# Optimization experiments

Measured on AMD Instinct MI355X. Metric: run time of the kernel, lower is better.

## Reference

```python
import jax, jax.numpy as jnp
import numpy as np

NPOINT = 2048
RADIUS = 0.2
NSAMPLE = 64
BN_EPS = 1e-5
MLP = [131, 128, 128, 256]  # 128 features + 3 xyz -> 128 -> 128 -> 256


def fps(xyz, npoint):
    """Furthest point sampling. xyz: (B,N,3) -> inds (B,npoint) int32. First index is 0 (CUDA convention)."""
    B, N, _ = xyz.shape
    dist0 = jnp.full((B, N), 1e10, dtype=xyz.dtype)
    idx0 = jnp.zeros((B,), dtype=jnp.int32)

    def step(carry, _):
        dist, last = carry
        last_pt = jnp.take_along_axis(xyz, last[:, None, None].astype(jnp.int32), axis=1)  # (B,1,3)
        d = jnp.sum((xyz - last_pt) ** 2, axis=-1)  # (B,N)
        dist = jnp.minimum(dist, d)
        nxt = jnp.argmax(dist, axis=1).astype(jnp.int32)
        return (dist, nxt), nxt

    (_, _), rest = jax.lax.scan(step, (dist0, idx0), None, length=npoint - 1)
    return jnp.concatenate([idx0[None, :], rest], axis=0).T  # (B,npoint)


def ball_query(all_xyz, new_xyz, radius, nsample):
    """For each query pick the first (lowest-index) nsample points within radius; pad with first hit.
    all_xyz: (B,Np,3), new_xyz: (B,S,3) -> idx (B,S,nsample) int32."""
    Np = all_xyz.shape[1]
    d2 = jnp.sum((new_xyz[:, :, None, :] - all_xyz[:, None, :, :]) ** 2, axis=-1)  # (B,S,Np)
    key = jnp.where(d2 < radius * radius, jnp.arange(Np, dtype=jnp.int32)[None, None, :], Np)
    topk = -jax.lax.top_k(-key, nsample)[0]  # nsample smallest indices, ascending
    valid = topk < Np
    first = topk[..., :1]
    idx = jnp.where(valid, topk, first)
    return jnp.where(idx >= Np, 0, idx).astype(jnp.int32)


def bn_relu(x, gamma, beta):
    # training-mode BatchNorm over (B,S,K) per channel (last axis), biased variance
    mean = jnp.mean(x, axis=(0, 1, 2), keepdims=True)
    var = jnp.mean((x - mean) ** 2, axis=(0, 1, 2), keepdims=True)
    return jax.nn.relu((x - mean) * jax.lax.rsqrt(var + BN_EPS) * gamma + beta)


def setup_inputs() -> dict:
    key = jax.random.key(0)
    ks = jax.random.split(key, 10)
    B, N, M, C = 4, 16384, 256, 128
    fixed_xyz = jax.random.uniform(ks[0], (B, M, 3), dtype=jnp.float32)
    xyz = jax.random.uniform(ks[1], (B, N, 3), dtype=jnp.float32)
    features = jax.random.normal(ks[2], (B, C, M + N), dtype=jnp.float32)
    W1 = jax.random.normal(ks[3], (MLP[1], MLP[0]), dtype=jnp.float32) * 0.05
    W2 = jax.random.normal(ks[4], (MLP[2], MLP[1]), dtype=jnp.float32) * 0.05
    W3 = jax.random.normal(ks[5], (MLP[3], MLP[2]), dtype=jnp.float32) * 0.05
    g1 = jnp.ones((MLP[1],), jnp.float32); b1 = jnp.zeros((MLP[1],), jnp.float32)
    g2 = jnp.ones((MLP[2],), jnp.float32); b2 = jnp.zeros((MLP[2],), jnp.float32)
    g3 = jnp.ones((MLP[3],), jnp.float32); b3 = jnp.zeros((MLP[3],), jnp.float32)
    return {"fixed_xyz": fixed_xyz, "xyz": xyz, "features": features,
            "W1": W1, "g1": g1, "b1": b1, "W2": W2, "g2": g2, "b2": b2,
            "W3": W3, "g3": g3, "b3": b3}


def reference(fixed_xyz, xyz, features, W1, g1, b1, W2, g2, b2, W3, g3, b3):
    B = xyz.shape[0]
    # FPS on the raw cloud, gather sampled centers, prepend fixed seeds
    inds = fps(xyz, NPOINT)  # (B,npoint)
    sampled = jnp.take_along_axis(xyz, inds[:, :, None], axis=1)  # (B,npoint,3)
    new_xyz = jnp.concatenate([fixed_xyz, sampled], axis=1)       # (B,S,3)
    all_xyz = jnp.concatenate([fixed_xyz, xyz], axis=1)           # (B,Np,3)

    idx = ball_query(all_xyz, new_xyz, RADIUS, NSAMPLE)           # (B,S,K)
    b = jnp.arange(B)[:, None, None]
    grouped_xyz = all_xyz[b, idx] - new_xyz[:, :, None, :]        # (B,S,K,3)
    grouped_xyz = grouped_xyz / RADIUS                            # normalize_xyz=True
    feats_t = jnp.transpose(features, (0, 2, 1))                  # (B,Np,C)
    grouped_feats = feats_t[b, idx]                               # (B,S,K,C)
    h = jnp.concatenate([grouped_xyz, grouped_feats], axis=-1)    # (B,S,K,3+C)

    # Shared MLP: 1x1 conv (no bias) + BN + ReLU per layer
    h = bn_relu(jnp.einsum('bskc,oc->bsko', h, W1), g1, b1)
    h = bn_relu(jnp.einsum('bskc,oc->bsko', h, W2), g2, b2)
    h = bn_relu(jnp.einsum('bskc,oc->bsko', h, W3), g3, b3)

    # max pool over the K (nsample) axis -> (B,Cout,S)
    new_features = jnp.transpose(jnp.max(h, axis=2), (0, 2, 1))
    return new_xyz, new_features, inds
```

## Files before the change

kernel.cpp:

```cpp
#include <hip/hip_runtime.h>
#include <hip/hip_bf16.h>
#include <cstdint>
#include <cstddef>

#define NB 4
#define N_PTS 16384
#define M_FIX 256
#define P_ALL 16640
#define S_TOT 2304
#define NPT 2048
#define KNB 64
#define CH1 128
#define CH3 256
#define NRED 589824.0f

typedef float v2f __attribute__((ext_vector_type(2)));

#define OUT_XYZ 0
#define OUT_FEAT 27648
#define OUT_INDS 2386944

#define OFF_ALLX   0ull
#define OFF_STATS  798720ull
#define OFF_BN     1060864ull
#define OFF_MAXZ   1064960ull
#define OFF_MINZ   10502144ull
#define OFF_IDX    19939328ull
#define OFF_ZP     22298624ull
#define OFF_NEWX   39337984ull
#define OFF_INDSI  39448576ull
#define OFF_HIST   1064960ull
#define OFF_OFFS   1073152ull
#define OFF_SX     1081344ull
#define OFF_SY     1343488ull
#define OFF_SZ     1605632ull
#define OFF_SIDX   1867776ull
#define OFF_XYZ4   2129920ull

__device__ __forceinline__ float red16s(float v) {
  v += __shfl_xor(v, 1); v += __shfl_xor(v, 2);
  v += __shfl_xor(v, 4); v += __shfl_xor(v, 8);
  return v;
}
__device__ __forceinline__ float red16mx(float v) {
  v = fmaxf(v, __shfl_xor(v, 1)); v = fmaxf(v, __shfl_xor(v, 2));
  v = fmaxf(v, __shfl_xor(v, 4)); v = fmaxf(v, __shfl_xor(v, 8));
  return v;
}
__device__ __forceinline__ float red16mn(float v) {
  v = fminf(v, __shfl_xor(v, 1)); v = fminf(v, __shfl_xor(v, 2));
  v = fminf(v, __shfl_xor(v, 4)); v = fminf(v, __shfl_xor(v, 8));
  return v;
}
__device__ __forceinline__ float xyzp(float dx, float dy, float dz,
                                      float wx, float wy, float wz) {
  return fmaf(dx, wx, fmaf(dy, wy, __fmul_rn(dz, wz)));
}
__device__ __forceinline__ int mort3(int v) {
  return (v & 1) | ((v & 2) << 1) | ((v & 4) << 2);
}
__device__ __forceinline__ int cell_code(float x, float y, float z) {
  int cx = min(7, max(0, (int)(x * 8.0f)));
  int cy = min(7, max(0, (int)(y * 8.0f)));
  int cz = min(7, max(0, (int)(z * 8.0f)));
  return mort3(cx) | (mort3(cy) << 1) | (mort3(cz) << 2);
}

template <int CTRL, int RM>
__device__ __forceinline__ unsigned long long dppmax(unsigned long long k) {
  int lo = (int)(unsigned)(k & 0xFFFFFFFFull);
  int hi = (int)(unsigned)(k >> 32);
  int sl = __builtin_amdgcn_update_dpp(lo, lo, CTRL, RM, 0xF, false);
  int sh = __builtin_amdgcn_update_dpp(hi, hi, CTRL, RM, 0xF, false);
  unsigned long long s = ((unsigned long long)(unsigned)sh << 32) | (unsigned)sl;
  return (s > k) ? s : k;
}
__device__ __forceinline__ unsigned long long wave_max64(unsigned long long k) {
  k = dppmax<0x111, 0xF>(k);
  k = dppmax<0x112, 0xF>(k);
  k = dppmax<0x114, 0xF>(k);
  k = dppmax<0x118, 0xF>(k);
  k = dppmax<0x142, 0xa>(k);
  k = dppmax<0x143, 0xc>(k);
  return k;
}
__device__ __forceinline__ unsigned long long row_max64(unsigned long long k) {
  k = dppmax<0x111, 0xF>(k);
  k = dppmax<0x112, 0xF>(k);
  k = dppmax<0x114, 0xF>(k);
  k = dppmax<0x118, 0xF>(k);
  return k;
}

__global__ void k_build(const float* __restrict__ fixed, const float* __restrict__ xyz,
                        float* __restrict__ allx, float* __restrict__ newx,
                        float* __restrict__ stats, int* __restrict__ inds_i,
                        int* __restrict__ hist, float4* __restrict__ xyz4) {
  int i = blockIdx.x * 256 + threadIdx.x;
  if (i < NB * P_ALL * 3) {
    int b = i / (P_ALL * 3);
    int r = i % (P_ALL * 3);
    int p = r / 3, c = r % 3;
    float v = (p < M_FIX) ? fixed[((size_t)b * M_FIX + p) * 3 + c]
                          : xyz[((size_t)b * N_PTS + (p - M_FIX)) * 3 + c];
    allx[i] = v;
  }
  if (i < NB * N_PTS) {
    const float* pt = xyz + (size_t)i * 3;
    xyz4[i] = make_float4(pt[0], pt[1], pt[2], 0.f);
  }
  if (i < NB * M_FIX * 3) {
    int b = i / (M_FIX * 3);
    int r = i % (M_FIX * 3);
    newx[(size_t)b * S_TOT * 3 + r] = fixed[(size_t)b * M_FIX * 3 + r];
  }
  if (i < 65536) stats[i] = 0.0f;
  if (i < NB * 512) hist[i] = 0;
  if (i < NB) inds_i[(size_t)i * NPT] = 0;
}

__global__ void k_cell(const float* __restrict__ xyz, int* __restrict__ hist) {
  int i = blockIdx.x * 256 + threadIdx.x;
  int b = i >> 14;
  const float* pt = xyz + (size_t)i * 3;
  int code = cell_code(pt[0], pt[1], pt[2]);
  atomicAdd(&hist[(b << 9) + code], 1);
}

__global__ __launch_bounds__(512) void k_scan(const int* __restrict__ hist,
                                              int* __restrict__ offs) {
  __shared__ int tmp[512];
  int b = blockIdx.x, t = threadIdx.x;
  int h = hist[(b << 9) + t];
  tmp[t] = h;
  __syncthreads();
  for (int o = 1; o < 512; o <<= 1) {
    int v = (t >= o) ? tmp[t - o] : 0;
    __syncthreads();
    tmp[t] += v;
    __syncthreads();
  }
  offs[(b << 9) + t] = tmp[t] - h;
}

__global__ void k_scatter(const float* __restrict__ xyz, int* __restrict__ offs,
                          float* __restrict__ sx, float* __restrict__ sy,
                          float* __restrict__ sz, int* __restrict__ sidx) {
  int i = blockIdx.x * 256 + threadIdx.x;
  int b = i >> 14, p = i & 16383;
  const float* pt = xyz + (size_t)i * 3;
  float x = pt[0], y = pt[1], z = pt[2];
  int code = cell_code(x, y, z);
  int pos = atomicAdd(&offs[(b << 9) + code], 1);
  int o = (b << 14) + pos;
  sx[o] = x; sy[o] = y; sz[o] = z; sidx[o] = p;
}

__global__ __launch_bounds__(1024, 4) void k_fps(const float4* __restrict__ xyz4,
                                                 const float* __restrict__ sx,
                                                 const float* __restrict__ sy,
                                                 const float* __restrict__ sz,
                                                 const int* __restrict__ sidx,
                                                 float* __restrict__ newx,
                                                 int* __restrict__ inds_i) {
  int b = blockIdx.x, t = threadIdx.x;
  const float4* bx4 = xyz4 + (size_t)b * N_PTS;
  int off0 = (b << 14) + (t << 4);
  v2f px2[8], py2[8], pz2[8];
  float dist[16];
  unsigned npidp[8];
#pragma unroll
  for (int u = 0; u < 8; ++u) {
    px2[u] = *(const v2f*)&sx[off0 + 2 * u];
    py2[u] = *(const v2f*)&sy[off0 + 2 * u];
    pz2[u] = *(const v2f*)&sz[off0 + 2 * u];
    dist[2 * u] = 1e10f; dist[2 * u + 1] = 1e10f;
  }
#pragma unroll
  for (int u = 0; u < 8; ++u) {
    unsigned a = 16383u - (unsigned)sidx[off0 + 2 * u];
    unsigned c = 16383u - (unsigned)sidx[off0 + 2 * u + 1];
    npidp[u] = a | (c << 16);
  }
  float xmn = px2[0].x, xmx = px2[0].x, ymn = py2[0].x, ymx = py2[0].x;
  float zmn = pz2[0].x, zmx = pz2[0].x;
#pragma unroll
  for (int u = 0; u < 8; ++u) {
    xmn = fminf(xmn, fminf(px2[u].x, px2[u].y));
    xmx = fmaxf(xmx, fmaxf(px2[u].x, px2[u].y));
    ymn = fminf(ymn, fminf(py2[u].x, py2[u].y));
    ymx = fmaxf(ymx, fmaxf(py2[u].x, py2[u].y));
    zmn = fminf(zmn, fminf(pz2[u].x, pz2[u].y));
    zmx = fmaxf(zmx, fmaxf(pz2[u].x, pz2[u].y));
  }
  float cx = (xmn + xmx) * 0.5f, cy = (ymn + ymx) * 0.5f, cz = (zmn + zmx) * 0.5f;
  float r2m = 0.f;
#pragma unroll
  for (int u = 0; u < 8; ++u) {
#pragma unroll
    for (int h = 0; h < 2; ++h) {
      float ax = (h ? px2[u].y : px2[u].x) - cx;
      float ay = (h ? py2[u].y : py2[u].x) - cy;
      float az = (h ? pz2[u].y : pz2[u].x) - cz;
      r2m = fmaxf(r2m, ax * ax + ay * ay + az * az);
    }
  }
  float rad = sqrtf(r2m) + 2e-3f;
  float4 p0 = bx4[0];
  float lx = p0.x, ly = p0.y, lz = p0.z;
  if (t == 0) {
    size_t nb0 = ((size_t)b * S_TOT + M_FIX) * 3;
    newx[nb0] = lx; newx[nb0 + 1] = ly; newx[nb0 + 2] = lz;
  }
  __shared__ unsigned long long red[16];
  __shared__ __align__(16) float4 wcoord[16];
  __shared__ __align__(16) float4 s_win;
  __shared__ int idxbuf[NPT];
  unsigned long long bestkey = 0ull;
  unsigned long long kprev = ~0ull;
  float thr = 3.4e38f;
  int lane = t & 63, wid = t >> 6;
  for (int iter = 1; iter < NPT; ++iter) {
    float ex = lx - cx, ey = ly - cy, ez = lz - cz;
    bool active = (ex * ex + ey * ey + ez * ez) < thr;
    if (__ballot(active) != 0ull) {
      bool ch = false;
      if (active) {
#pragma clang fp contract(off)
        v2f l2x = {lx, lx}, l2y = {ly, ly}, l2z = {lz, lz};
#pragma unroll
        for (int u = 0; u < 8; ++u) {
          v2f dx = px2[u] - l2x;
          v2f dy = py2[u] - l2y;
          v2f dz = pz2[u] - l2z;
          v2f xx = dx * dx;
          v2f yy = dy * dy;
          v2f zz = dz * dz;
          v2f d2 = (xx + yy) + zz;
          if (d2.x < dist[2 * u])     { dist[2 * u] = d2.x;     ch = true; }
          if (d2.y < dist[2 * u + 1]) { dist[2 * u + 1] = d2.y; ch = true; }
        }
      }
      if (__ballot(ch) != 0ull) {
        if (ch) {
          unsigned long long c0 = 0ull, c1 = 0ull, c2 = 0ull, c3 = 0ull;
#pragma unroll
          for (int j = 0; j < 16; ++j) {
            unsigned lo16 = (j & 1) ? (npidp[j >> 1] >> 16) : (npidp[j >> 1] & 0xFFFFu);
            unsigned long long kj =
                ((unsigned long long)__float_as_uint(dist[j]) << 32) | lo16;
            if ((j & 3) == 0) c0 = (kj > c0) ? kj : c0;
            else if ((j & 3) == 1) c1 = (kj > c1) ? kj : c1;
            else if ((j & 3) == 2) c2 = (kj > c2) ? kj : c2;
            else c3 = (kj > c3) ? kj : c3;
          }
          c0 = (c1 > c0) ? c1 : c0;
          c2 = (c3 > c2) ? c3 : c2;
          bestkey = (c2 > c0) ? c2 : c0;
          float ub = __uint_as_float((unsigned)(bestkey >> 32));
          float tq = sqrtf(ub) + rad;
          thr = tq * tq;
        }
        unsigned long long k = wave_max64(bestkey);
        unsigned long long kall = __shfl(k, 63);
        if (kall != kprev) {
          if (bestkey == kall) {
            unsigned lo = (unsigned)(kall & 0xFFFFull);
            float wx = 0.f, wy = 0.f, wz = 0.f;
#pragma unroll
            for (int u = 0; u < 8; ++u) {
              unsigned pk = npidp[u];
              if ((pk & 0xFFFFu) == lo) { wx = px2[u].x; wy = py2[u].x; wz = pz2[u].x; }
              if ((pk >> 16) == lo)     { wx = px2[u].y; wy = py2[u].y; wz = pz2[u].y; }
            }
            wcoord[wid] = make_float4(wx, wy, wz, 0.f);
          }
          kprev = kall;
        }
        if (lane == 63) red[wid] = k;
      }
    }
    __syncthreads();
    if (wid == 0) {
      unsigned long long wk = red[lane & 15];
      unsigned long long wr = row_max64(wk);
      unsigned long long wmax = __shfl(wr, 15);
      unsigned long long mb = __ballot(wk == wmax) & 0xFFFFull;
      int src = __ffsll(mb) - 1;
      if (lane == 15) {
        s_win = wcoord[src];
        idxbuf[iter] = 16383 - (int)(wmax & 0xFFFFull);
      }
    }
    __syncthreads();
    float4 wv = s_win;
    lx = wv.x; ly = wv.y; lz = wv.z;
  }
  __syncthreads();
  for (int s = t; s < NPT; s += 1024) {
    if (s == 0) continue;
    int wi = idxbuf[s];
    float4 wp = bx4[wi];
    inds_i[(size_t)b * NPT + s] = wi;
    size_t nb2 = ((size_t)b * S_TOT + M_FIX + s) * 3;
    newx[nb2] = wp.x; newx[nb2 + 1] = wp.y; newx[nb2 + 2] = wp.z;
  }
}

__global__ __launch_bounds__(256) void k_ball(const float* __restrict__ allx,
                                              const float* __restrict__ newx,
                                              int* __restrict__ idx) {
  int wid = threadIdx.x >> 6, lane = threadIdx.x & 63;
  int q = blockIdx.x * 4 + wid;
  int b = q / S_TOT;
  const float* qp = newx + (size_t)q * 3;
  float qx = qp[0], qy = qp[1], qz = qp[2];
  const float* pts = allx + (size_t)b * P_ALL * 3;
  int* outp = idx + (size_t)q * KNB;
  const float R2 = 0.04f;
  int collected = 0;
  int first_hit = 0;
  for (int ch = 0; ch < P_ALL / 64; ++ch) {
    int p = ch * 64 + lane;
    float x = pts[p * 3 + 0], y = pts[p * 3 + 1], z = pts[p * 3 + 2];
    float dx = __fsub_rn(qx, x), dy = __fsub_rn(qy, y), dz = __fsub_rn(qz, z);
    float d2 = __fadd_rn(__fadd_rn(__fmul_rn(dx, dx), __fmul_rn(dy, dy)), __fmul_rn(dz, dz));
    bool hit = d2 < R2;
    unsigned long long m = __ballot(hit);
    if (m) {
      if (collected == 0) first_hit = ch * 64 + (__ffsll((unsigned long long)m) - 1);
      if (hit) {
        int slot = collected + __popcll(m & ((1ull << lane) - 1ull));
        if (slot < KNB) outp[slot] = p;
      }
      collected += __popcll(m);
      if (collected >= KNB) break;
    }
  }
  int sl = collected + lane;
  if (sl < KNB) outp[sl] = first_hit;
}

__device__ __forceinline__ void gemm_chunks(const float* a_t, float* w_t,
                                            const float* __restrict__ Wg, int K,
                                            int obase, int ldw, int tid,
                                            float acc[4][8]) {
  int tk = tid & 15, to = tid >> 4;
  for (int c0 = 0; c0 < K; c0 += 32) {
    __syncthreads();
    for (int r = tid; r < 32 * 128; r += 256) {
      int o = r & 127, c = r >> 7;
      w_t[c * 132 + o] = Wg[(size_t)(obase + o) * ldw + (c0 + c)];
    }
    __syncthreads();
#pragma unroll 4
    for (int c = 0; c < 32; ++c) {
      float a4[4], w8[8];
      *(float4*)a4 = *(const float4*)&a_t[(c0 + c) * 68 + tk * 4];
      *(float4*)w8 = *(const float4*)&w_t[c * 132 + to * 8];
      *(float4*)(w8 + 4) = *(const float4*)&w_t[c * 132 + to * 8 + 4];
#pragma unroll
      for (int i = 0; i < 4; ++i)
#pragma unroll
        for (int j = 0; j < 8; ++j) acc[i][j] = fmaf(a4[i], w8[j], acc[i][j]);
    }
  }
}

__global__ __launch_bounds__(256) void k_zp(const float* __restrict__ feats,
                                            const float* __restrict__ W1,
                                            __hip_bfloat16* __restrict__ zp) {
  __shared__ __align__(16) float smem[CH1 * 68 + 32 * 132];
  float* a_t = smem;
  float* w_t = smem + CH1 * 68;
  int b = blockIdx.y;
  int p0 = blockIdx.x * 64;
  int tid = threadIdx.x;
  for (int r = tid; r < CH1 * 64; r += 256) {
    int c = r >> 6, p = r & 63;
    a_t[c * 68 + p] = feats[((size_t)b * CH1 + c) * P_ALL + p0 + p];
  }
  float acc[4][8];
#pragma unroll
  for (int i = 0; i < 4; ++i)
#pragma unroll
    for (int j = 0; j < 8; ++j) acc[i][j] = 0.f;
  gemm_chunks(a_t, w_t, W1 + 3, CH1, 0, 131, tid, acc);
  int tk = tid & 15, to = tid >> 4;
#pragma unroll
  for (int i = 0; i < 4; ++i) {
    int p = p0 + tk * 4 + i;
    union { __hip_bfloat16 h[8]; uint4 u; } tmp;
#pragma unroll
    for (int j = 0; j < 8; ++j) tmp.h[j] = __float2bfloat16(acc[i][j]);
    *(uint4*)&zp[((size_t)b * P_ALL + p) * CH1 + to * 8] = tmp.u;
  }
}

__device__ __forceinline__ void stage_geom(int bs, int b, const int* __restrict__ idxg,
                                           const float* __restrict__ allx,
                                           const float* __restrict__ newx,
                                           const float* __restrict__ W1,
                                           int* s_pid, float* s_d, float* s_w1, int tid) {
  if (tid < 64) {
    int p = idxg[(size_t)bs * KNB + tid];
    s_pid[tid] = p;
    const float* pp = allx + ((size_t)b * P_ALL + p) * 3;
    const float* qq = newx + (size_t)bs * 3;
    s_d[tid]       = __fmul_rn(__fsub_rn(pp[0], qq[0]), 5.0f);
    s_d[64 + tid]  = __fmul_rn(__fsub_rn(pp[1], qq[1]), 5.0f);
    s_d[128 + tid] = __fmul_rn(__fsub_rn(pp[2], qq[2]), 5.0f);
  } else if (tid < 192) {
    int c = tid - 64;
    s_w1[c]       = W1[(size_t)c * 131 + 0];
    s_w1[128 + c] = W1[(size_t)c * 131 + 1];
    s_w1[256 + c] = W1[(size_t)c * 131 + 2];
  }
  __syncthreads();
}

__global__ __launch_bounds__(256) void k_stats1(const int* __restrict__ idxg,
                                                const float* __restrict__ allx,
                                                const float* __restrict__ newx,
                                                const float* __restrict__ W1,
                                                const __hip_bfloat16* __restrict__ zp,
                                                float* __restrict__ sSum,
                                                float* __restrict__ sSq) {
  __shared__ float smem[640 + 512];
  int* s_pid = (int*)smem;
  float* s_d = smem + 64;
  float* s_w1 = smem + 256;
  float* red = smem + 640;
  int bs = blockIdx.x;
  int b = bs / S_TOT;
  int tid = threadIdx.x;
  stage_geom(bs, b, idxg, allx, newx, W1, s_pid, s_d, s_w1, tid);
  int g = tid >> 7, c = tid & 127;
  float wx = s_w1[c], wy = s_w1[128 + c], wz = s_w1[256 + c];
  const uint16_t* zpb = (const uint16_t*)zp + (size_t)b * P_ALL * CH1;
  float s1 = 0.f, s2 = 0.f;
  for (int k = g; k < KNB; k += 2) {
    int pid = s_pid[k];
    float v = __uint_as_float(((unsigned)zpb[(size_t)pid * CH1 + c]) << 16);
    v += xyzp(s_d[k], s_d[64 + k], s_d[128 + k], wx, wy, wz);
    s1 += v; s2 = fmaf(v, v, s2);
  }
  red[tid] = s1;
  __syncthreads();
  float t1 = (tid < 128) ? red[tid] + red[tid + 128] : 0.f;
  __syncthreads();
  red[tid] = s2;
  __syncthreads();
  if (tid < 128) {
    float t2 = red[tid] + red[tid + 128];
    int slot = bs & 63;
    atomicAdd(&sSum[slot * CH1 + tid], t1);
    atomicAdd(&sSq[slot * CH1 + tid], t2);
  }
}

__device__ __forceinline__ void build_a1(float* a_t, const int* s_pid, const float* s_d,
                                         const float* s_w1,
                                         const __hip_bfloat16* __restrict__ zp_b,
                                         const float* __restrict__ bnS,
                                         const float* __restrict__ bnH, int tid) {
  int k = tid >> 2, q = tid & 3;
  int pid = s_pid[k];
  float dx = s_d[k], dy = s_d[64 + k], dz = s_d[128 + k];
  const uint32_t* zr = (const uint32_t*)((const uint16_t*)zp_b + (size_t)pid * CH1 + q * 32);
#pragma unroll
  for (int u = 0; u < 16; ++u) {
    uint32_t w = zr[u];
    int c = q * 32 + u * 2;
    float v0 = __uint_as_float(w << 16);
    float v1 = __uint_as_float(w & 0xFFFF0000u);
    v0 += xyzp(dx, dy, dz, s_w1[c], s_w1[128 + c], s_w1[256 + c]);
    v1 += xyzp(dx, dy, dz, s_w1[c + 1], s_w1[128 + c + 1], s_w1[256 + c + 1]);
    a_t[c * 68 + k]       = fmaxf(fmaf(v0, bnS[c], bnH[c]), 0.0f);
    a_t[(c + 1) * 68 + k] = fmaxf(fmaf(v1, bnS[c + 1], bnH[c + 1]), 0.0f);
  }
}

__global__ __launch_bounds__(256) void k_layer2s(const int* __restrict__ idxg,
                                                 const float* __restrict__ allx,
                                                 const float* __restrict__ newx,
                                                 const float* __restrict__ W1,
                                                 const __hip_bfloat16* __restrict__ zp,
                                                 const float* __restrict__ bn1S,
                                                 const float* __restrict__ bn1H,
                                                 const float* __restrict__ W2,
                                                 float* __restrict__ sSum,
                                                 float* __restrict__ sSq) {
  __shared__ __align__(16) float smem[CH1 * 68 + 32 * 132];
  float* a_t = smem;
  float* w_t = smem + CH1 * 68;
  int* s_pid = (int*)w_t;
  float* s_d = w_t + 64;
  float* s_w1 = w_t + 256;
  int bs = blockIdx.x;
  int b = bs / S_TOT;
  int tid = threadIdx.x;
  stage_geom(bs, b, idxg, allx, newx, W1, s_pid, s_d, s_w1, tid);
  build_a1(a_t, s_pid, s_d, s_w1, zp + (size_t)b * P_ALL * CH1, bn1S, bn1H, tid);
  float acc[4][8];
#pragma unroll
  for (int i = 0; i < 4; ++i)
#pragma unroll
    for (int j = 0; j < 8; ++j) acc[i][j] = 0.f;
  gemm_chunks(a_t, w_t, W2, CH1, 0, CH1, tid, acc);
  int tk = tid & 15, to = tid >> 4;
  int slot = bs & 63;
#pragma unroll
  for (int j = 0; j < 8; ++j) {
    float s1 = 0.f, s2 = 0.f;
#pragma unroll
    for (int i = 0; i < 4; ++i) { float v = acc[i][j]; s1 += v; s2 = fmaf(v, v, s2); }
    s1 = red16s(s1);
    s2 = red16s(s2);
    if (tk == 0) {
      int o = to * 8 + j;
      atomicAdd(&sSum[slot * CH1 + o], s1);
      atomicAdd(&sSq[slot * CH1 + o], s2);
    }
  }
}

__global__ __launch_bounds__(256) void k_layer3(const int* __restrict__ idxg,
                                                const float* __restrict__ allx,
                                                const float* __restrict__ newx,
                                                const float* __restrict__ W1,
                                                const __hip_bfloat16* __restrict__ zp,
                                                const float* __restrict__ bn1S,
                                                const float* __restrict__ bn1H,
                                                const float* __restrict__ W2,
                                                const float* __restrict__ bn2S,
                                                const float* __restrict__ bn2H,
                                                const float* __restrict__ W3,
                                                float* __restrict__ maxz,
                                                float* __restrict__ minz,
                                                float* __restrict__ sSum,
                                                float* __restrict__ sSq) {
  __shared__ __align__(16) float smem[CH1 * 68 + 32 * 132];
  float* a_t = smem;
  float* w_t = smem + CH1 * 68;
  int* s_pid = (int*)w_t;
  float* s_d = w_t + 64;
  float* s_w1 = w_t + 256;
  int bs = blockIdx.x;
  int b = bs / S_TOT;
  int tid = threadIdx.x;
  stage_geom(bs, b, idxg, allx, newx, W1, s_pid, s_d, s_w1, tid);
  build_a1(a_t, s_pid, s_d, s_w1, zp + (size_t)b * P_ALL * CH1, bn1S, bn1H, tid);
  float acc[4][8];
#pragma unroll
  for (int i = 0; i < 4; ++i)
#pragma unroll
    for (int j = 0; j < 8; ++j) acc[i][j] = 0.f;
  gemm_chunks(a_t, w_t, W2, CH1, 0, CH1, tid, acc);
  int tk = tid & 15, to = tid >> 4;
  __syncthreads();
#pragma unroll
  for (int j = 0; j < 8; ++j) {
    int o = to * 8 + j;
    float sc = bn2S[o], sh = bn2H[o];
#pragma unroll
    for (int i = 0; i < 4; ++i)
      a_t[o * 68 + tk * 4 + i] = fmaxf(fmaf(acc[i][j], sc, sh), 0.0f);
  }
  int slot = bs & 63;
#pragma unroll 1
  for (int half = 0; half < 2; ++half) {
    float acc3[4][8];
#pragma unroll
    for (int i = 0; i < 4; ++i)
#pragma unroll
      for (int j = 0; j < 8; ++j) acc3[i][j] = 0.f;
    gemm_chunks(a_t, w_t, W3, CH1, half * 128, CH1, tid, acc3);
#pragma unroll
    for (int j = 0; j < 8; ++j) {
      float s1 = 0.f, s2 = 0.f, mx = -3.4e38f, mn = 3.4e38f;
#pragma unroll
      for (int i = 0; i < 4; ++i) {
        float v = acc3[i][j];
        s1 += v; s2 = fmaf(v, v, s2);
        mx = fmaxf(mx, v); mn = fminf(mn, v);
      }
      s1 = red16s(s1);
      s2 = red16s(s2);
      mx = red16mx(mx);
      mn = red16mn(mn);
      if (tk == 0) {
        int o = half * 128 + to * 8 + j;
        atomicAdd(&sSum[slot * CH3 + o], s1);
        atomicAdd(&sSq[slot * CH3 + o], s2);
        size_t base = (size_t)bs * CH3 + o;
        maxz[base] = mx;
        minz[base] = mn;
      }
    }
  }
}

__global__ void k_fin(const float* __restrict__ sSum, const float* __restrict__ sSq,
                      const float* __restrict__ gamma, const float* __restrict__ beta,
                      float* __restrict__ bnS, float* __restrict__ bnH, int C) {
  int o = threadIdx.x;
  if (o >= C) return;
  float s1 = 0.f, s2 = 0.f;
  for (int t = 0; t < 64; ++t) { s1 += sSum[t * C + o]; s2 += sSq[t * C + o]; }
  float mean = s1 / NRED;
  float var = fmaxf(s2 / NRED - mean * mean, 0.f);
  float inv = 1.0f / sqrtf(var + 1e-5f);
  float sc = gamma[o] * inv;
  bnS[o] = sc;
  bnH[o] = beta[o] - mean * sc;
}

__global__ __launch_bounds__(256) void k_final(const float* __restrict__ maxz,
                                               const float* __restrict__ minz,
                                               const float* __restrict__ bnS,
                                               const float* __restrict__ bnH,
                                               float* __restrict__ out) {
  int bs = blockIdx.x;
  int o = threadIdx.x;
  float sc = bnS[o], sh = bnH[o];
  size_t base = (size_t)bs * CH3 + o;
  float v = (sc >= 0.f) ? maxz[base] : minz[base];
  float r = fmaxf(fmaf(v, sc, sh), 0.f);
  int b = bs / S_TOT, s = bs % S_TOT;
  out[OUT_FEAT + ((size_t)b * CH3 + o) * S_TOT + s] = r;
}

__global__ void k_copy(const float* __restrict__ newx, const int* __restrict__ inds_i,
                       float* __restrict__ out) {
  int i = blockIdx.x * 256 + threadIdx.x;
  if (i < NB * S_TOT * 3) out[OUT_XYZ + i] = newx[i];
  else {
    int r = i - NB * S_TOT * 3;
    if (r < NB * NPT) out[OUT_INDS + r] = (float)inds_i[r];
  }
}

extern "C" void kernel_launch(void* const* d_in, const int* in_sizes, int n_in,
                              void* d_out, int out_size, void* d_ws, size_t ws_size,
                              hipStream_t stream) {
  const float* fixed = (const float*)d_in[0];
  const float* xyz = (const float*)d_in[1];
  const float* feats = (const float*)d_in[2];
  const float* W1 = (const float*)d_in[3];
  const float* g1 = (const float*)d_in[4];
  const float* b1 = (const float*)d_in[5];
  const float* W2 = (const float*)d_in[6];
  const float* g2 = (const float*)d_in[7];
  const float* b2 = (const float*)d_in[8];
  const float* W3 = (const float*)d_in[9];
  const float* g3 = (const float*)d_in[10];
  const float* b3 = (const float*)d_in[11];
  float* out = (float*)d_out;

  char* w = (char*)d_ws;
  float* allx = (float*)(w + OFF_ALLX);
  float* newx = (float*)(w + OFF_NEWX);
  int* inds_i = (int*)(w + OFF_INDSI);
  int* idx = (int*)(w + OFF_IDX);
  float* stats = (float*)(w + OFF_STATS);
  float* s1sum = stats, *s1sq = stats + 8192;
  float* s2sum = stats + 16384, *s2sq = stats + 24576;
  float* s3sum = stats + 32768, *s3sq = stats + 49152;
  float* bn = (float*)(w + OFF_BN);
  float* bn1s = bn, *bn1h = bn + 128;
  float* bn2s = bn + 256, *bn2h = bn + 384;
  float* bn3s = bn + 512, *bn3h = bn + 768;
  float* maxz = (float*)(w + OFF_MAXZ);
  float* minz = (float*)(w + OFF_MINZ);
  __hip_bfloat16* zp = (__hip_bfloat16*)(w + OFF_ZP);
  int* hist = (int*)(w + OFF_HIST);
  int* offs = (int*)(w + OFF_OFFS);
  float* sxp = (float*)(w + OFF_SX);
  float* syp = (float*)(w + OFF_SY);
  float* szp = (float*)(w + OFF_SZ);
  int* sidx = (int*)(w + OFF_SIDX);
  float4* xyz4 = (float4*)(w + OFF_XYZ4);

  k_build<<<(NB * P_ALL * 3 + 255) / 256, 256, 0, stream>>>(fixed, xyz, allx, newx, stats, inds_i, hist, xyz4);
  k_cell<<<NB * N_PTS / 256, 256, 0, stream>>>(xyz, hist);
  k_scan<<<NB, 512, 0, stream>>>(hist, offs);
  k_scatter<<<NB * N_PTS / 256, 256, 0, stream>>>(xyz, offs, sxp, syp, szp, sidx);
  k_fps<<<NB, 1024, 0, stream>>>(xyz4, sxp, syp, szp, sidx, newx, inds_i);
  k_ball<<<(NB * S_TOT) / 4, 256, 0, stream>>>(allx, newx, idx);
  k_zp<<<dim3(P_ALL / 64, NB), 256, 0, stream>>>(feats, W1, zp);
  k_stats1<<<NB * S_TOT, 256, 0, stream>>>(idx, allx, newx, W1, zp, s1sum, s1sq);
  k_fin<<<1, 256, 0, stream>>>(s1sum, s1sq, g1, b1, bn1s, bn1h, 128);
  k_layer2s<<<NB * S_TOT, 256, 0, stream>>>(idx, allx, newx, W1, zp, bn1s, bn1h, W2, s2sum, s2sq);
  k_fin<<<1, 256, 0, stream>>>(s2sum, s2sq, g2, b2, bn2s, bn2h, 128);
  k_layer3<<<NB * S_TOT, 256, 0, stream>>>(idx, allx, newx, W1, zp, bn1s, bn1h, W2,
                                           bn2s, bn2h, W3, maxz, minz, s3sum, s3sq);
  k_fin<<<1, 256, 0, stream>>>(s3sum, s3sq, g3, b3, bn3s, bn3h, 256);
  k_final<<<NB * S_TOT, 256, 0, stream>>>(maxz, minz, bn3s, bn3h, out);
  k_copy<<<(NB * S_TOT * 3 + NB * NPT + 255) / 256, 256, 0, stream>>>(newx, inds_i, out);
}
```

Before: 4.829 ms.

## Use packed FP32 FMA in shared GEMM and remap build_a1 thread layout

The inner GEMM accumulator is switched to 2-wide float vectors so the compiler can emit packed FP32 FMA instructions (v_pk_fma_f32), which halves the number of FMA instructions in the register-blocked 4x8 microkernel. All epilogues read the accumulators through an index macro. Separately, build_a1 now maps threads as k = tid&63, q = tid>>6 instead of k = tid>>2, which changes both the gather pattern over zp rows and the LDS write pattern into a_t. That second change may shift bank conflicts and global coalescing either way.

```diff
diff --git a/kernel.cpp b/kernel.cpp
--- a/kernel.cpp
+++ b/kernel.cpp
@@ -344,7 +344,7 @@
 __device__ __forceinline__ void gemm_chunks(const float* a_t, float* w_t,
                                             const float* __restrict__ Wg, int K,
                                             int obase, int ldw, int tid,
-                                            float acc[4][8]) {
+                                            v2f acc[4][4]) {
   int tk = tid & 15, to = tid >> 4;
   for (int c0 = 0; c0 < K; c0 += 32) {
     __syncthreads();
@@ -355,17 +355,22 @@
     __syncthreads();
 #pragma unroll 4
     for (int c = 0; c < 32; ++c) {
-      float a4[4], w8[8];
+      float a4[4];
+      v2f w2[4];
       *(float4*)a4 = *(const float4*)&a_t[(c0 + c) * 68 + tk * 4];
-      *(float4*)w8 = *(const float4*)&w_t[c * 132 + to * 8];
-      *(float4*)(w8 + 4) = *(const float4*)&w_t[c * 132 + to * 8 + 4];
-#pragma unroll
-      for (int i = 0; i < 4; ++i)
-#pragma unroll
-        for (int j = 0; j < 8; ++j) acc[i][j] = fmaf(a4[i], w8[j], acc[i][j]);
+      *(float4*)&w2[0] = *(const float4*)&w_t[c * 132 + to * 8];
+      *(float4*)&w2[2] = *(const float4*)&w_t[c * 132 + to * 8 + 4];
+#pragma unroll
+      for (int i = 0; i < 4; ++i) {
+        v2f a2 = {a4[i], a4[i]};
+#pragma unroll
+        for (int p = 0; p < 4; ++p)
+          acc[i][p] = __builtin_elementwise_fma(a2, w2[p], acc[i][p]);
+      }
     }
   }
 }
+#define ACC_J(acc, i, j) (((j) & 1) ? acc[i][(j) >> 1].y : acc[i][(j) >> 1].x)
 
 __global__ __launch_bounds__(256) void k_zp(const float* __restrict__ feats,
                                             const float* __restrict__ W1,
@@ -380,11 +385,11 @@
     int c = r >> 6, p = r & 63;
     a_t[c * 68 + p] = feats[((size_t)b * CH1 + c) * P_ALL + p0 + p];
   }
-  float acc[4][8];
+  v2f acc[4][4];
 #pragma unroll
   for (int i = 0; i < 4; ++i)
 #pragma unroll
-    for (int j = 0; j < 8; ++j) acc[i][j] = 0.f;
+    for (int p = 0; p < 4; ++p) acc[i][p] = (v2f){0.f, 0.f};
   gemm_chunks(a_t, w_t, W1 + 3, CH1, 0, 131, tid, acc);
   int tk = tid & 15, to = tid >> 4;
 #pragma unroll
@@ -392,7 +397,7 @@
     int p = p0 + tk * 4 + i;
     union { __hip_bfloat16 h[8]; uint4 u; } tmp;
 #pragma unroll
-    for (int j = 0; j < 8; ++j) tmp.h[j] = __float2bfloat16(acc[i][j]);
+    for (int j = 0; j < 8; ++j) tmp.h[j] = __float2bfloat16(ACC_J(acc, i, j));
     *(uint4*)&zp[((size_t)b * P_ALL + p) * CH1 + to * 8] = tmp.u;
   }
 }
@@ -464,7 +469,7 @@
                                          const __hip_bfloat16* __restrict__ zp_b,
                                          const float* __restrict__ bnS,
                                          const float* __restrict__ bnH, int tid) {
-  int k = tid >> 2, q = tid & 3;
+  int k = tid & 63, q = tid >> 6;
   int pid = s_pid[k];
   float dx = s_d[k], dy = s_d[64 + k], dz = s_d[128 + k];
   const uint32_t* zr = (const uint32_t*)((const uint16_t*)zp_b + (size_t)pid * CH1 + q * 32);
@@ -502,11 +507,11 @@
   int tid = threadIdx.x;
   stage_geom(bs, b, idxg, allx, newx, W1, s_pid, s_d, s_w1, tid);
   build_a1(a_t, s_pid, s_d, s_w1, zp + (size_t)b * P_ALL * CH1, bn1S, bn1H, tid);
-  float acc[4][8];
+  v2f acc[4][4];
 #pragma unroll
   for (int i = 0; i < 4; ++i)
 #pragma unroll
-    for (int j = 0; j < 8; ++j) acc[i][j] = 0.f;
+    for (int p = 0; p < 4; ++p) acc[i][p] = (v2f){0.f, 0.f};
   gemm_chunks(a_t, w_t, W2, CH1, 0, CH1, tid, acc);
   int tk = tid & 15, to = tid >> 4;
   int slot = bs & 63;
@@ -514,7 +519,7 @@
   for (int j = 0; j < 8; ++j) {
     float s1 = 0.f, s2 = 0.f;
 #pragma unroll
-    for (int i = 0; i < 4; ++i) { float v = acc[i][j]; s1 += v; s2 = fmaf(v, v, s2); }
+    for (int i = 0; i < 4; ++i) { float v = ACC_J(acc, i, j); s1 += v; s2 = fmaf(v, v, s2); }
     s1 = red16s(s1);
     s2 = red16s(s2);
     if (tk == 0) {
@@ -551,11 +556,11 @@
   int tid = threadIdx.x;
   stage_geom(bs, b, idxg, allx, newx, W1, s_pid, s_d, s_w1, tid);
   build_a1(a_t, s_pid, s_d, s_w1, zp + (size_t)b * P_ALL * CH1, bn1S, bn1H, tid);
-  float acc[4][8];
+  v2f acc[4][4];
 #pragma unroll
   for (int i = 0; i < 4; ++i)
 #pragma unroll
-    for (int j = 0; j < 8; ++j) acc[i][j] = 0.f;
+    for (int p = 0; p < 4; ++p) acc[i][p] = (v2f){0.f, 0.f};
   gemm_chunks(a_t, w_t, W2, CH1, 0, CH1, tid, acc);
   int tk = tid & 15, to = tid >> 4;
   __syncthreads();
@@ -565,23 +570,23 @@
     float sc = bn2S[o], sh = bn2H[o];
 #pragma unroll
     for (int i = 0; i < 4; ++i)
-      a_t[o * 68 + tk * 4 + i] = fmaxf(fmaf(acc[i][j], sc, sh), 0.0f);
+      a_t[o * 68 + tk * 4 + i] = fmaxf(fmaf(ACC_J(acc, i, j), sc, sh), 0.0f);
   }
   int slot = bs & 63;
 #pragma unroll 1
   for (int half = 0; half < 2; ++half) {
-    float acc3[4][8];
+    v2f acc3[4][4];
 #pragma unroll
     for (int i = 0; i < 4; ++i)
 #pragma unroll
-      for (int j = 0; j < 8; ++j) acc3[i][j] = 0.f;
+      for (int p = 0; p < 4; ++p) acc3[i][p] = (v2f){0.f, 0.f};
     gemm_chunks(a_t, w_t, W3, CH1, half * 128, CH1, tid, acc3);
 #pragma unroll
     for (int j = 0; j < 8; ++j) {
       float s1 = 0.f, s2 = 0.f, mx = -3.4e38f, mn = 3.4e38f;
 #pragma unroll
       for (int i = 0; i < 4; ++i) {
-        float v = acc3[i][j];
+        float v = ACC_J(acc3, i, j);
         s1 += v; s2 = fmaf(v, v, s2);
         mx = fmaxf(mx, v); mn = fminf(mn, v);
       }
```

Result: faster. 4.645 ms (-3.8%).
